# Kernel optimization log

Hardware: AMD Instinct MI355X
Metric: run time of the kernel (lower is better)

Reference implementation:

```python
import jax, jax.numpy as jnp
import numpy as np

N_NODES = 50000
N_EDGES = 800000
IN_FEAT = 128
HEADS = 8
HEAD_DIM = 16  # out_feat // num_heads = 128 // 8
NEG_SLOPE = 0.2


def setup_inputs() -> dict:
    key = jax.random.key(0)
    ks = jax.random.split(key, 8)
    g = 1.0 / np.sqrt(IN_FEAT)
    return {
        "x": jax.random.normal(ks[0], (N_NODES, IN_FEAT), jnp.float32),
        "efeat": jax.random.normal(ks[1], (N_EDGES, IN_FEAT), jnp.float32),
        "src": jax.random.randint(ks[2], (N_EDGES,), 0, N_NODES),
        "dst": jax.random.randint(ks[3], (N_EDGES,), 0, N_NODES),
        "W_src": jax.random.normal(ks[4], (HEADS * HEAD_DIM, IN_FEAT), jnp.float32) * g,
        "b_src": jnp.zeros((HEADS * HEAD_DIM,), jnp.float32),
        "W_dst": jax.random.normal(ks[5], (HEADS * HEAD_DIM, IN_FEAT), jnp.float32) * g,
        "b_dst": jnp.zeros((HEADS * HEAD_DIM,), jnp.float32),
        "W_edge": jax.random.normal(ks[6], (HEADS * HEAD_DIM, IN_FEAT), jnp.float32) * g,
        "attn": jax.random.normal(ks[7], (HEADS, HEAD_DIM), jnp.float32) * (1.0 / np.sqrt(HEAD_DIM)),
    }


def reference(x, efeat, src, dst, W_src, b_src, W_dst, b_dst, W_edge, attn):
    H, D = HEADS, HEAD_DIM
    # node/edge projections: [N,H,D] / [E,H,D]
    feat_src = (x @ W_src.T + b_src).reshape(-1, H, D)
    feat_dst = (x @ W_dst.T + b_dst).reshape(-1, H, D)
    feat_edge = (efeat @ W_edge.T).reshape(-1, H, D)

    # per-edge GATv2 score: LeakyReLU(src + dst + edge) . attn  -> [E,H]
    fs = feat_src[src]                                    # gather [E,H,D]
    tmp = fs + feat_dst[dst] + feat_edge
    e = jnp.where(tmp >= 0, tmp, NEG_SLOPE * tmp)
    score = jnp.einsum('ehd,hd->eh', e, attn)

    # edge softmax normalized per destination node
    m = jax.ops.segment_max(score, dst, num_segments=N_NODES)     # [N,H]
    ex = jnp.exp(score - jax.lax.stop_gradient(m)[dst])
    z = jax.ops.segment_sum(ex, dst, num_segments=N_NODES)        # [N,H]
    a = ex / z[dst]                                               # [E,H]

    # weighted scatter-sum of (src + edge) messages
    msg = (fs + feat_edge) * a[:, :, None]                        # [E,H,D]
    h = jax.ops.segment_sum(msg, dst, num_segments=N_NODES)       # [N,H,D]

    # res_fc is None since in_feat == H*D; activation = relu
    h = jax.nn.relu(h)
    return h.reshape(N_NODES, H * D)
```

## Files before the change

### kernel.cpp

```cpp
#include <hip/hip_runtime.h>
#include <hip/hip_bf16.h>

#define NNODES 50000
#define NEDGES 800000
#define NEG_SLOPE 0.2f
#define N_PAD 50176

typedef float f32x4 __attribute__((ext_vector_type(4)));
typedef float f32x2 __attribute__((ext_vector_type(2)));
typedef __bf16 bf16x8 __attribute__((ext_vector_type(8)));
typedef __bf16 bf16x4 __attribute__((ext_vector_type(4)));
typedef __bf16 bf16x2 __attribute__((ext_vector_type(2)));

template<int OUT_BF16, int HAS_BIAS, int SCATTER>
__global__ __launch_bounds__(256, 2) void gemm_proj(
    const float* __restrict__ A, const float* __restrict__ W,
    const float* __restrict__ bias, const int* __restrict__ rank,
    void* __restrict__ outp, int M)
{
  __shared__ __bf16 sA[128*128];
  __shared__ __bf16 sB[128*128];
  const int t = threadIdx.x;
  const int m0 = blockIdx.x * 128;

  #pragma unroll
  for (int it = 0; it < 16; ++it){
    int lin = it*1024 + t*4;
    int r = lin >> 7, cx = lin & 127;
    f32x4 v = {0.f, 0.f, 0.f, 0.f};
    int gr = m0 + r;
    if (gr < M) v = *(const f32x4*)(A + (size_t)gr*128 + cx);
    int kb = cx >> 3, ko = cx & 7;
    int off = r*128 + ((kb ^ (r & 15)) << 3) + ko;
    bf16x4 pk = { (__bf16)v.x, (__bf16)v.y, (__bf16)v.z, (__bf16)v.w };
    *(bf16x4*)(sA + off) = pk;
  }
  #pragma unroll
  for (int it = 0; it < 16; ++it){
    int lin = it*1024 + t*4;
    int r = lin >> 7, cx = lin & 127;
    f32x4 v = *(const f32x4*)(W + lin);
    int kb = cx >> 3, ko = cx & 7;
    int off = r*128 + ((kb ^ (r & 15)) << 3) + ko;
    bf16x4 pk = { (__bf16)v.x, (__bf16)v.y, (__bf16)v.z, (__bf16)v.w };
    *(bf16x4*)(sB + off) = pk;
  }
  __syncthreads();

  const int w = t >> 6, lane = t & 63;
  const int rsel = lane & 15, quad = lane >> 4;
  f32x4 acc[2][8];
  f32x4 zero = {0.f, 0.f, 0.f, 0.f};
  #pragma unroll
  for (int mi = 0; mi < 2; ++mi)
    #pragma unroll
    for (int ni = 0; ni < 8; ++ni) acc[mi][ni] = zero;

  #pragma unroll
  for (int kk = 0; kk < 4; ++kk){
    int kb0 = kk*4 + quad;
    bf16x8 af[2], bf[8];
    #pragma unroll
    for (int mi = 0; mi < 2; ++mi){
      int r = w*32 + mi*16 + rsel;
      af[mi] = *(const bf16x8*)(sA + r*128 + ((kb0 ^ (r & 15)) << 3));
    }
    #pragma unroll
    for (int ni = 0; ni < 8; ++ni){
      int r = ni*16 + rsel;
      bf[ni] = *(const bf16x8*)(sB + r*128 + ((kb0 ^ (r & 15)) << 3));
    }
    #pragma unroll
    for (int mi = 0; mi < 2; ++mi)
      #pragma unroll
      for (int ni = 0; ni < 8; ++ni)
        acc[mi][ni] = __builtin_amdgcn_mfma_f32_16x16x32_bf16(af[mi], bf[ni], acc[mi][ni], 0, 0, 0);
  }

  int orow[2][4];
  #pragma unroll
  for (int mi = 0; mi < 2; ++mi)
    #pragma unroll
    for (int r4 = 0; r4 < 4; ++r4){
      int grow = m0 + w*32 + mi*16 + quad*4 + r4;
      orow[mi][r4] = (SCATTER && grow < M) ? rank[grow] : grow;
    }

  #pragma unroll
  for (int mi = 0; mi < 2; ++mi){
    #pragma unroll
    for (int ni = 0; ni < 8; ++ni){
      #pragma unroll
      for (int r4 = 0; r4 < 4; ++r4){
        int grow = m0 + w*32 + mi*16 + quad*4 + r4;
        int col = ni*16 + rsel;
        if (grow < M){
          float v = acc[mi][ni][r4];
          if (HAS_BIAS) v += bias[col];
          if (OUT_BF16) ((__bf16*)outp)[(size_t)orow[mi][r4]*128 + col] = (__bf16)v;
          else          ((float*)outp)[(size_t)orow[mi][r4]*128 + col] = v;
        }
      }
    }
  }
}

__global__ void hist_kernel(const int* __restrict__ dst, int* __restrict__ deg){
  int e = blockIdx.x*256 + threadIdx.x;
  atomicAdd(&deg[dst[e]], 1);
}

__global__ void scan_local(const int* __restrict__ deg, int* __restrict__ scanned,
                           int* __restrict__ bsum){
  __shared__ int s[1024];
  int t = threadIdx.x, i = blockIdx.x*1024 + t;
  int v = deg[i];
  s[t] = v; __syncthreads();
  #pragma unroll
  for (int off = 1; off < 1024; off <<= 1){
    int x = (t >= off) ? s[t-off] : 0;
    __syncthreads();
    s[t] += x;
    __syncthreads();
  }
  scanned[i] = s[t] - v;
  if (t == 1023) bsum[blockIdx.x] = s[t];
}

__global__ void scan_sums(int* __restrict__ bsum){
  __shared__ int s[64];
  int t = threadIdx.x;
  int v = (t < 49) ? bsum[t] : 0;
  s[t] = v; __syncthreads();
  #pragma unroll
  for (int off = 1; off < 64; off <<= 1){
    int x = (t >= off) ? s[t-off] : 0;
    __syncthreads();
    s[t] += x;
    __syncthreads();
  }
  bsum[t] = s[t] - v;
}

__global__ void scan_add(const int* __restrict__ scanned, const int* __restrict__ bsum,
                         int* __restrict__ row_start, int* __restrict__ cursor){
  int i = blockIdx.x*256 + threadIdx.x;
  if (i < N_PAD){
    int val = scanned[i] + bsum[i >> 10];
    row_start[i] = val;
    cursor[i] = val;
  }
}

__global__ void scatter_kernel(const int* __restrict__ dst, const int* __restrict__ src,
                               int* __restrict__ cursor, int* __restrict__ rank,
                               int* __restrict__ src_perm){
  int e = blockIdx.x*256 + threadIdx.x;
  int pos = atomicAdd(&cursor[dst[e]], 1);
  rank[e] = pos;
  src_perm[pos] = src[e];
}

__global__ __launch_bounds__(256) void aggregate_fused(
    const int* __restrict__ row_start, const int* __restrict__ deg,
    const int* __restrict__ src_perm, const float* __restrict__ fs,
    const float* __restrict__ fd, const __bf16* __restrict__ fe,
    const float* __restrict__ attn, float* __restrict__ out)
{
  int wv = threadIdx.x >> 6, lane = threadIdx.x & 63;
  int n = blockIdx.x*4 + wv;
  int row = row_start[n], dg = deg[n];
  int c = lane << 1;
  f32x2 fdv = *(const f32x2*)(fd + (size_t)n*128 + c);
  f32x2 atv = *(const f32x2*)(attn + c);
  float acc0 = 0.f, acc1 = 0.f, zs = 0.f;
  for (int base = 0; base < dg; base += 64){
    int cnt = min(64, dg - base);
    int si = 0;
    if (lane < cnt) si = src_perm[row + base + lane];
    for (int j = 0; j < cnt; ++j){
      int s = __shfl(si, j, 64);
      f32x2 fsv = *(const f32x2*)(fs + (size_t)s*128 + c);
      bf16x2 fev = *(const bf16x2*)(fe + (size_t)(row + base + j)*128 + c);
      float v0 = fsv.x + (float)fev.x;
      float v1 = fsv.y + (float)fev.y;
      float t0 = v0 + fdv.x; t0 = t0 >= 0.f ? t0 : NEG_SLOPE*t0;
      float t1 = v1 + fdv.y; t1 = t1 >= 0.f ? t1 : NEG_SLOPE*t1;
      float p = t0*atv.x + t1*atv.y;
      p += __shfl_xor(p, 1);
      p += __shfl_xor(p, 2);
      p += __shfl_xor(p, 4);
      float ex = __expf(p);
      acc0 += ex*v0; acc1 += ex*v1; zs += ex;
    }
  }
  float rz = zs > 0.f ? 1.f/zs : 0.f;
  float o0 = acc0*rz, o1 = acc1*rz;
  f32x2 ov = { o0 > 0.f ? o0 : 0.f, o1 > 0.f ? o1 : 0.f };
  *(f32x2*)(out + (size_t)n*128 + c) = ov;
}

extern "C" void kernel_launch(void* const* d_in, const int* in_sizes, int n_in,
                              void* d_out, int out_size, void* d_ws, size_t ws_size,
                              hipStream_t stream)
{
  const float* x      = (const float*)d_in[0];
  const float* efeat  = (const float*)d_in[1];
  const int*   src    = (const int*)d_in[2];
  const int*   dst    = (const int*)d_in[3];
  const float* W_src  = (const float*)d_in[4];
  const float* b_src  = (const float*)d_in[5];
  const float* W_dst  = (const float*)d_in[6];
  const float* b_dst  = (const float*)d_in[7];
  const float* W_edge = (const float*)d_in[8];
  const float* attn   = (const float*)d_in[9];

  char* ws = (char*)d_ws;
  float*  feat_src  = (float*)(ws + 0);
  float*  feat_dst  = (float*)(ws + 25600000);
  __bf16* fe        = (__bf16*)(ws + 51200000);
  int*    src_perm  = (int*)  (ws + 256000000);
  int*    rank      = (int*)  (ws + 259200000);
  int*    row_start = (int*)  (ws + 262400000);
  int*    cursor    = (int*)  (ws + 262600704);
  int*    scanned   = (int*)  (ws + 262801408);
  int*    deg       = (int*)  (ws + 263002112);
  int*    bsum      = (int*)  (ws + 263202816);

  hipMemsetAsync(deg, 0, 200704, stream);

  hist_kernel   <<<3125, 256, 0, stream>>>(dst, deg);
  scan_local    <<<49, 1024, 0, stream>>>(deg, scanned, bsum);
  scan_sums     <<<1, 64, 0, stream>>>(bsum);
  scan_add      <<<196, 256, 0, stream>>>(scanned, bsum, row_start, cursor);
  scatter_kernel<<<3125, 256, 0, stream>>>(dst, src, cursor, rank, src_perm);

  gemm_proj<0,1,0><<<391, 256, 0, stream>>>(x, W_src, b_src, nullptr, feat_src, NNODES);
  gemm_proj<0,1,0><<<391, 256, 0, stream>>>(x, W_dst, b_dst, nullptr, feat_dst, NNODES);
  gemm_proj<1,0,1><<<6250, 256, 0, stream>>>(efeat, W_edge, nullptr, rank, fe, NEDGES);

  aggregate_fused<<<12500, 256, 0, stream>>>(row_start, deg, src_perm, feat_src,
                                             feat_dst, fe, attn, (float*)d_out);
}
```

Before: 900.0 us.

## Pre-swizzle bf16 weights, load A fragments directly, drop scatter atomics, unroll aggregation

A new kernel converts all three weight matrices to swizzled bf16 once, so each GEMM block only copies weights into shared memory. A fragments now go straight from global memory into registers, removing the sA shared buffer and its extra pass. The histogram kernel records each edge's slot, so the scatter step drops its second atomic pass and the cursor array. The aggregation inner loop is unrolled by four to keep more gathers in flight. The direct A loads are less coalesced than the old staged loads, which may cost some bandwidth.

```diff
diff --git a/kernel.cpp b/kernel.cpp
--- a/kernel.cpp
+++ b/kernel.cpp
@@ -12,43 +12,58 @@
 typedef __bf16 bf16x4 __attribute__((ext_vector_type(4)));
 typedef __bf16 bf16x2 __attribute__((ext_vector_type(2)));
 
+__global__ __launch_bounds__(256) void convert_w3(
+    const float* __restrict__ W0, const float* __restrict__ W1,
+    const float* __restrict__ W2, __bf16* __restrict__ out)
+{
+  int m = blockIdx.x >> 4;
+  const float* W = (m == 0) ? W0 : ((m == 1) ? W1 : W2);
+  __bf16* o = out + m * 16384;
+  int i = (blockIdx.x & 15) * 1024 + threadIdx.x * 4;
+  int r = i >> 7, cx = i & 127;
+  f32x4 v = *(const f32x4*)(W + i);
+  int kb = cx >> 3, ko = cx & 7;
+  int off = r * 128 + ((kb ^ (r & 15)) << 3) + ko;
+  bf16x4 pk = { (__bf16)v.x, (__bf16)v.y, (__bf16)v.z, (__bf16)v.w };
+  *(bf16x4*)(o + off) = pk;
+}
+
 template<int OUT_BF16, int HAS_BIAS, int SCATTER>
 __global__ __launch_bounds__(256, 2) void gemm_proj(
-    const float* __restrict__ A, const float* __restrict__ W,
+    const float* __restrict__ A, const __bf16* __restrict__ Wsw,
     const float* __restrict__ bias, const int* __restrict__ rank,
     void* __restrict__ outp, int M)
 {
-  __shared__ __bf16 sA[128*128];
-  __shared__ __bf16 sB[128*128];
+  __shared__ __bf16 sB[128 * 128];
   const int t = threadIdx.x;
   const int m0 = blockIdx.x * 128;
 
   #pragma unroll
-  for (int it = 0; it < 16; ++it){
-    int lin = it*1024 + t*4;
-    int r = lin >> 7, cx = lin & 127;
-    f32x4 v = {0.f, 0.f, 0.f, 0.f};
-    int gr = m0 + r;
-    if (gr < M) v = *(const f32x4*)(A + (size_t)gr*128 + cx);
-    int kb = cx >> 3, ko = cx & 7;
-    int off = r*128 + ((kb ^ (r & 15)) << 3) + ko;
-    bf16x4 pk = { (__bf16)v.x, (__bf16)v.y, (__bf16)v.z, (__bf16)v.w };
-    *(bf16x4*)(sA + off) = pk;
-  }
-  #pragma unroll
-  for (int it = 0; it < 16; ++it){
-    int lin = it*1024 + t*4;
-    int r = lin >> 7, cx = lin & 127;
-    f32x4 v = *(const f32x4*)(W + lin);
-    int kb = cx >> 3, ko = cx & 7;
-    int off = r*128 + ((kb ^ (r & 15)) << 3) + ko;
-    bf16x4 pk = { (__bf16)v.x, (__bf16)v.y, (__bf16)v.z, (__bf16)v.w };
-    *(bf16x4*)(sB + off) = pk;
-  }
-  __syncthreads();
+  for (int it = 0; it < 8; ++it) {
+    int lin = it * 2048 + t * 8;
+    *(bf16x8*)(sB + lin) = *(const bf16x8*)(Wsw + lin);
+  }
 
   const int w = t >> 6, lane = t & 63;
   const int rsel = lane & 15, quad = lane >> 4;
+
+  bf16x8 af[4][2];
+  #pragma unroll
+  for (int mi = 0; mi < 2; ++mi) {
+    int gr = m0 + w * 32 + mi * 16 + rsel;
+    #pragma unroll
+    for (int kk = 0; kk < 4; ++kk) {
+      f32x4 v0 = {0.f, 0.f, 0.f, 0.f}, v1 = {0.f, 0.f, 0.f, 0.f};
+      if (gr < M) {
+        const float* p = A + (size_t)gr * 128 + kk * 32 + quad * 8;
+        v0 = *(const f32x4*)p;
+        v1 = *(const f32x4*)(p + 4);
+      }
+      af[kk][mi] = (bf16x8){ (__bf16)v0.x, (__bf16)v0.y, (__bf16)v0.z, (__bf16)v0.w,
+                             (__bf16)v1.x, (__bf16)v1.y, (__bf16)v1.z, (__bf16)v1.w };
+    }
+  }
+
   f32x4 acc[2][8];
   f32x4 zero = {0.f, 0.f, 0.f, 0.f};
   #pragma unroll
@@ -56,69 +71,67 @@
     #pragma unroll
     for (int ni = 0; ni < 8; ++ni) acc[mi][ni] = zero;
 
-  #pragma unroll
-  for (int kk = 0; kk < 4; ++kk){
-    int kb0 = kk*4 + quad;
-    bf16x8 af[2], bf[8];
-    #pragma unroll
-    for (int mi = 0; mi < 2; ++mi){
-      int r = w*32 + mi*16 + rsel;
-      af[mi] = *(const bf16x8*)(sA + r*128 + ((kb0 ^ (r & 15)) << 3));
-    }
-    #pragma unroll
-    for (int ni = 0; ni < 8; ++ni){
-      int r = ni*16 + rsel;
-      bf[ni] = *(const bf16x8*)(sB + r*128 + ((kb0 ^ (r & 15)) << 3));
+  __syncthreads();
+
+  #pragma unroll
+  for (int kk = 0; kk < 4; ++kk) {
+    int kb0 = kk * 4 + quad;
+    bf16x8 bfr[8];
+    #pragma unroll
+    for (int ni = 0; ni < 8; ++ni) {
+      int r = ni * 16 + rsel;
+      bfr[ni] = *(const bf16x8*)(sB + r * 128 + ((kb0 ^ (r & 15)) << 3));
     }
     #pragma unroll
     for (int mi = 0; mi < 2; ++mi)
       #pragma unroll
       for (int ni = 0; ni < 8; ++ni)
-        acc[mi][ni] = __builtin_amdgcn_mfma_f32_16x16x32_bf16(af[mi], bf[ni], acc[mi][ni], 0, 0, 0);
+        acc[mi][ni] = __builtin_amdgcn_mfma_f32_16x16x32_bf16(af[kk][mi], bfr[ni], acc[mi][ni], 0, 0, 0);
   }
 
   int orow[2][4];
   #pragma unroll
   for (int mi = 0; mi < 2; ++mi)
     #pragma unroll
-    for (int r4 = 0; r4 < 4; ++r4){
-      int grow = m0 + w*32 + mi*16 + quad*4 + r4;
+    for (int r4 = 0; r4 < 4; ++r4) {
+      int grow = m0 + w * 32 + mi * 16 + quad * 4 + r4;
       orow[mi][r4] = (SCATTER && grow < M) ? rank[grow] : grow;
     }
 
   #pragma unroll
-  for (int mi = 0; mi < 2; ++mi){
-    #pragma unroll
-    for (int ni = 0; ni < 8; ++ni){
+  for (int mi = 0; mi < 2; ++mi) {
+    #pragma unroll
+    for (int ni = 0; ni < 8; ++ni) {
       #pragma unroll
-      for (int r4 = 0; r4 < 4; ++r4){
-        int grow = m0 + w*32 + mi*16 + quad*4 + r4;
-        int col = ni*16 + rsel;
-        if (grow < M){
+      for (int r4 = 0; r4 < 4; ++r4) {
+        int grow = m0 + w * 32 + mi * 16 + quad * 4 + r4;
+        int col = ni * 16 + rsel;
+        if (grow < M) {
           float v = acc[mi][ni][r4];
           if (HAS_BIAS) v += bias[col];
-          if (OUT_BF16) ((__bf16*)outp)[(size_t)orow[mi][r4]*128 + col] = (__bf16)v;
-          else          ((float*)outp)[(size_t)orow[mi][r4]*128 + col] = v;
+          if (OUT_BF16) ((__bf16*)outp)[(size_t)orow[mi][r4] * 128 + col] = (__bf16)v;
+          else          ((float*)outp)[(size_t)orow[mi][r4] * 128 + col] = v;
         }
       }
     }
   }
 }
 
-__global__ void hist_kernel(const int* __restrict__ dst, int* __restrict__ deg){
-  int e = blockIdx.x*256 + threadIdx.x;
-  atomicAdd(&deg[dst[e]], 1);
+__global__ void hist_kernel(const int* __restrict__ dst, int* __restrict__ deg,
+                            int* __restrict__ arr){
+  int e = blockIdx.x * 256 + threadIdx.x;
+  arr[e] = atomicAdd(&deg[dst[e]], 1);
 }
 
 __global__ void scan_local(const int* __restrict__ deg, int* __restrict__ scanned,
                            int* __restrict__ bsum){
   __shared__ int s[1024];
-  int t = threadIdx.x, i = blockIdx.x*1024 + t;
+  int t = threadIdx.x, i = blockIdx.x * 1024 + t;
   int v = deg[i];
   s[t] = v; __syncthreads();
   #pragma unroll
   for (int off = 1; off < 1024; off <<= 1){
-    int x = (t >= off) ? s[t-off] : 0;
+    int x = (t >= off) ? s[t - off] : 0;
     __syncthreads();
     s[t] += x;
     __syncthreads();
@@ -134,7 +147,7 @@
   s[t] = v; __syncthreads();
   #pragma unroll
   for (int off = 1; off < 64; off <<= 1){
-    int x = (t >= off) ? s[t-off] : 0;
+    int x = (t >= off) ? s[t - off] : 0;
     __syncthreads();
     s[t] += x;
     __syncthreads();
@@ -143,20 +156,16 @@
 }
 
 __global__ void scan_add(const int* __restrict__ scanned, const int* __restrict__ bsum,
-                         int* __restrict__ row_start, int* __restrict__ cursor){
-  int i = blockIdx.x*256 + threadIdx.x;
-  if (i < N_PAD){
-    int val = scanned[i] + bsum[i >> 10];
-    row_start[i] = val;
-    cursor[i] = val;
-  }
+                         int* __restrict__ row_start){
+  int i = blockIdx.x * 256 + threadIdx.x;
+  if (i < N_PAD) row_start[i] = scanned[i] + bsum[i >> 10];
 }
 
 __global__ void scatter_kernel(const int* __restrict__ dst, const int* __restrict__ src,
-                               int* __restrict__ cursor, int* __restrict__ rank,
+                               const int* __restrict__ row_start, int* __restrict__ rank,
                                int* __restrict__ src_perm){
-  int e = blockIdx.x*256 + threadIdx.x;
-  int pos = atomicAdd(&cursor[dst[e]], 1);
+  int e = blockIdx.x * 256 + threadIdx.x;
+  int pos = row_start[dst[e]] + rank[e];
   rank[e] = pos;
   src_perm[pos] = src[e];
 }
@@ -168,36 +177,64 @@
     const float* __restrict__ attn, float* __restrict__ out)
 {
   int wv = threadIdx.x >> 6, lane = threadIdx.x & 63;
-  int n = blockIdx.x*4 + wv;
+  int n = blockIdx.x * 4 + wv;
   int row = row_start[n], dg = deg[n];
   int c = lane << 1;
-  f32x2 fdv = *(const f32x2*)(fd + (size_t)n*128 + c);
+  f32x2 fdv = *(const f32x2*)(fd + (size_t)n * 128 + c);
   f32x2 atv = *(const f32x2*)(attn + c);
   float acc0 = 0.f, acc1 = 0.f, zs = 0.f;
+  const __bf16* fep = fe + (size_t)row * 128 + c;
+
+  #define EDGE_BODY(FV, EV)                                            \
+    {                                                                  \
+      float v0 = (FV).x + (float)(EV).x;                               \
+      float v1 = (FV).y + (float)(EV).y;                               \
+      float t0 = v0 + fdv.x; t0 = t0 >= 0.f ? t0 : NEG_SLOPE * t0;     \
+      float t1 = v1 + fdv.y; t1 = t1 >= 0.f ? t1 : NEG_SLOPE * t1;     \
+      float p = t0 * atv.x + t1 * atv.y;                               \
+      p += __shfl_xor(p, 1);                                           \
+      p += __shfl_xor(p, 2);                                           \
+      p += __shfl_xor(p, 4);                                           \
+      float ex = __expf(p);                                            \
+      acc0 += ex * v0; acc1 += ex * v1; zs += ex;                      \
+    }
+
   for (int base = 0; base < dg; base += 64){
     int cnt = min(64, dg - base);
     int si = 0;
     if (lane < cnt) si = src_perm[row + base + lane];
-    for (int j = 0; j < cnt; ++j){
-      int s = __shfl(si, j, 64);
-      f32x2 fsv = *(const f32x2*)(fs + (size_t)s*128 + c);
-      bf16x2 fev = *(const bf16x2*)(fe + (size_t)(row + base + j)*128 + c);
-      float v0 = fsv.x + (float)fev.x;
-      float v1 = fsv.y + (float)fev.y;
-      float t0 = v0 + fdv.x; t0 = t0 >= 0.f ? t0 : NEG_SLOPE*t0;
-      float t1 = v1 + fdv.y; t1 = t1 >= 0.f ? t1 : NEG_SLOPE*t1;
-      float p = t0*atv.x + t1*atv.y;
-      p += __shfl_xor(p, 1);
-      p += __shfl_xor(p, 2);
-      p += __shfl_xor(p, 4);
-      float ex = __expf(p);
-      acc0 += ex*v0; acc1 += ex*v1; zs += ex;
-    }
-  }
-  float rz = zs > 0.f ? 1.f/zs : 0.f;
-  float o0 = acc0*rz, o1 = acc1*rz;
+    int j = 0;
+    for (; j + 4 <= cnt; j += 4){
+      int s0 = __shfl(si, j,     64);
+      int s1 = __shfl(si, j + 1, 64);
+      int s2 = __shfl(si, j + 2, 64);
+      int s3 = __shfl(si, j + 3, 64);
+      f32x2 f0 = *(const f32x2*)(fs + (size_t)s0 * 128 + c);
+      f32x2 f1 = *(const f32x2*)(fs + (size_t)s1 * 128 + c);
+      f32x2 f2 = *(const f32x2*)(fs + (size_t)s2 * 128 + c);
+      f32x2 f3 = *(const f32x2*)(fs + (size_t)s3 * 128 + c);
+      bf16x2 e0 = *(const bf16x2*)(fep + (size_t)(base + j)     * 128);
+      bf16x2 e1 = *(const bf16x2*)(fep + (size_t)(base + j + 1) * 128);
+      bf16x2 e2 = *(const bf16x2*)(fep + (size_t)(base + j + 2) * 128);
+      bf16x2 e3 = *(const bf16x2*)(fep + (size_t)(base + j + 3) * 128);
+      EDGE_BODY(f0, e0)
+      EDGE_BODY(f1, e1)
+      EDGE_BODY(f2, e2)
+      EDGE_BODY(f3, e3)
+    }
+    for (; j < cnt; ++j){
+      int s0 = __shfl(si, j, 64);
+      f32x2 f0 = *(const f32x2*)(fs + (size_t)s0 * 128 + c);
+      bf16x2 e0 = *(const bf16x2*)(fep + (size_t)(base + j) * 128);
+      EDGE_BODY(f0, e0)
+    }
+  }
+  #undef EDGE_BODY
+
+  float rz = zs > 0.f ? 1.f / zs : 0.f;
+  float o0 = acc0 * rz, o1 = acc1 * rz;
   f32x2 ov = { o0 > 0.f ? o0 : 0.f, o1 > 0.f ? o1 : 0.f };
-  *(f32x2*)(out + (size_t)n*128 + c) = ov;
+  *(f32x2*)(out + (size_t)n * 128 + c) = ov;
 }
 
 extern "C" void kernel_launch(void* const* d_in, const int* in_sizes, int n_in,
@@ -222,22 +259,24 @@
   int*    src_perm  = (int*)  (ws + 256000000);
   int*    rank      = (int*)  (ws + 259200000);
   int*    row_start = (int*)  (ws + 262400000);
-  int*    cursor    = (int*)  (ws + 262600704);
   int*    scanned   = (int*)  (ws + 262801408);
   int*    deg       = (int*)  (ws + 263002112);
   int*    bsum      = (int*)  (ws + 263202816);
+  __bf16* wsw       = (__bf16*)(ws + 263203840);
 
   hipMemsetAsync(deg, 0, 200704, stream);
 
-  hist_kernel   <<<3125, 256, 0, stream>>>(dst, deg);
+  convert_w3<<<48, 256, 0, stream>>>(W_src, W_dst, W_edge, wsw);
+
+  hist_kernel   <<<3125, 256, 0, stream>>>(dst, deg, rank);
   scan_local    <<<49, 1024, 0, stream>>>(deg, scanned, bsum);
   scan_sums     <<<1, 64, 0, stream>>>(bsum);
-  scan_add      <<<196, 256, 0, stream>>>(scanned, bsum, row_start, cursor);
-  scatter_kernel<<<3125, 256, 0, stream>>>(dst, src, cursor, rank, src_perm);
-
-  gemm_proj<0,1,0><<<391, 256, 0, stream>>>(x, W_src, b_src, nullptr, feat_src, NNODES);
-  gemm_proj<0,1,0><<<391, 256, 0, stream>>>(x, W_dst, b_dst, nullptr, feat_dst, NNODES);
-  gemm_proj<1,0,1><<<6250, 256, 0, stream>>>(efeat, W_edge, nullptr, rank, fe, NEDGES);
+  scan_add      <<<196, 256, 0, stream>>>(scanned, bsum, row_start);
+  scatter_kernel<<<3125, 256, 0, stream>>>(dst, src, row_start, rank, src_perm);
+
+  gemm_proj<0,1,0><<<391, 256, 0, stream>>>(x, wsw,           b_src, nullptr, feat_src, NNODES);
+  gemm_proj<0,1,0><<<391, 256, 0, stream>>>(x, wsw + 16384,   b_dst, nullptr, feat_dst, NNODES);
+  gemm_proj<1,0,1><<<6250, 256, 0, stream>>>(efeat, wsw + 32768, nullptr, rank, fe, NEDGES);
 
   aggregate_fused<<<12500, 256, 0, stream>>>(row_start, deg, src_perm, feat_src,
                                              feat_dst, fe, attn, (float*)d_out);
```

Result: faster. 782.4 us (-13.1%).
